# Optimization experiments

Hardware: AMD Instinct MI355X
Metric: run time of the kernel (lower is better)

The kernel has to match this reference:

```python
import jax, jax.numpy as jnp
import numpy as np

POOL = (7, 7)          # pool_size from init
CROP = (14, 14)        # crop_size = [p*2 for p in pool_size]


def setup_inputs() -> dict:
    key = jax.random.key(0)
    kf, kxy, kwh = jax.random.split(key, 3)
    H_img, W_img = 800, 800
    feature = jax.random.normal(kf, (1, 50, 50, 512), dtype=jnp.float32)
    N = 1024
    # valid boxes: x1<x2, y1<y2, inside the 800x800 image
    xy1 = jax.random.uniform(kxy, (N, 2), minval=0.0, maxval=600.0)
    wh = jax.random.uniform(kwh, (N, 2), minval=32.0, maxval=200.0)
    xy2 = jnp.clip(xy1 + wh, 0.0, 799.0)
    rois = jnp.concatenate([xy1[:, 0:1], xy1[:, 1:2], xy2[:, 0:1], xy2[:, 1:2]], axis=1)  # (x1,y1,x2,y2)
    img_size = jnp.array([H_img, W_img], dtype=jnp.int32)  # (H, W)
    return {"feature": feature, "rois": rois, "img_size": img_size}


def _roi_pool(feature, rois, img_size):
    H, W = feature.shape[1], feature.shape[2]
    ch, cw = CROP
    ih = img_size[0].astype(jnp.float32)
    iw = img_size[1].astype(jnp.float32)
    # normalize rois (x1,y1,x2,y2) by [W,H,W,H], reorder to (y1,x1,y2,x2)
    x1 = rois[:, 0] / iw
    y1 = rois[:, 1] / ih
    x2 = rois[:, 2] / iw
    y2 = rois[:, 3] / ih
    # TF crop_and_resize sampling grid (crop size > 1 branch)
    gy = jnp.arange(ch, dtype=jnp.float32)
    gx = jnp.arange(cw, dtype=jnp.float32)
    in_y = y1[:, None] * (H - 1) + gy[None, :] * ((y2 - y1) * (H - 1) / (ch - 1))[:, None]  # [N,ch]
    in_x = x1[:, None] * (W - 1) + gx[None, :] * ((x2 - x1) * (W - 1) / (cw - 1))[:, None]  # [N,cw]
    top = jnp.floor(in_y)
    left = jnp.floor(in_x)
    ly = in_y - top   # [N,ch]
    lx = in_x - left  # [N,cw]
    t = jnp.clip(top, 0, H - 1).astype(jnp.int32)
    b = jnp.clip(top + 1, 0, H - 1).astype(jnp.int32)
    l = jnp.clip(left, 0, W - 1).astype(jnp.int32)
    r = jnp.clip(left + 1, 0, W - 1).astype(jnp.int32)
    img = feature[0]  # box_ind is all zeros -> single image [H,W,C]
    tl = img[t[:, :, None], l[:, None, :]]  # [N,ch,cw,C]
    tr = img[t[:, :, None], r[:, None, :]]
    bl = img[b[:, :, None], l[:, None, :]]
    br = img[b[:, :, None], r[:, None, :]]
    lyE = ly[:, :, None, None]
    lxE = lx[:, None, :, None]
    crops = (tl * (1 - lyE) * (1 - lxE) + tr * (1 - lyE) * lxE
             + bl * lyE * (1 - lxE) + br * lyE * lxE)
    # extrapolation_value = 0 outside [0, dim-1]
    valid = (((in_y >= 0) & (in_y <= H - 1))[:, :, None]
             & ((in_x >= 0) & (in_x <= W - 1))[:, None, :])
    crops = jnp.where(valid[..., None], crops, 0.0)
    # 2x2 max pool, stride 2 (crop dims are even so SAME == VALID)
    N, C = crops.shape[0], crops.shape[-1]
    pooled = crops.reshape(N, ch // 2, 2, cw // 2, 2, C).max(axis=(2, 4))  # [N,7,7,C]
    return pooled


def reference(feature, rois, img_size):
    return _roi_pool(feature, rois, img_size)
```

## Files before the change

kernel.cpp:

```cpp
#include <hip/hip_runtime.h>

#define FH 50
#define FW 50
#define FC 512
#define NROI 1024
#define ROWBYTES (FW * FC * 4)
#define COLBYTES (FC * 4)

typedef float f4v __attribute__((ext_vector_type(4)));

__device__ __forceinline__ float uflane(float v) {
    return __int_as_float(__builtin_amdgcn_readfirstlane(__float_as_int(v)));
}

__device__ __forceinline__ float4 lerp4(float4 a, float4 b, float t) {
    float4 r;
    r.x = fmaf(t, b.x - a.x, a.x);
    r.y = fmaf(t, b.y - a.y, a.y);
    r.z = fmaf(t, b.z - a.z, a.z);
    r.w = fmaf(t, b.w - a.w, a.w);
    return r;
}

__device__ __forceinline__ float4 max44(float4 a, float4 b) {
    float4 r;
    r.x = fmaxf(a.x, b.x);
    r.y = fmaxf(a.y, b.y);
    r.z = fmaxf(a.z, b.z);
    r.w = fmaxf(a.w, b.w);
    return r;
}

__global__ __launch_bounds__(256, 6) void roi_pool_kernel(
    const float* __restrict__ feature,
    const float* __restrict__ rois,
    const int*   __restrict__ img_size,
    float*       __restrict__ out)
{
    int tid  = threadIdx.x;
    int wid  = (blockIdx.x * 256 + tid) >> 6;
    wid = __builtin_amdgcn_readfirstlane(wid);
    int lane = tid & 63;

    int n    = wid / 14;
    int rem  = wid - n * 14;
    int py   = rem >> 1;
    int half = rem & 1;

    float ih = (float)__builtin_amdgcn_readfirstlane(img_size[0]);
    float iw = (float)__builtin_amdgcn_readfirstlane(img_size[1]);
    const float* rp = rois + (size_t)n * 4;
    float x1 = uflane(rp[0]) / iw;
    float y1 = uflane(rp[1]) / ih;
    float x2 = uflane(rp[2]) / iw;
    float y2 = uflane(rp[3]) / ih;

    const float HM1 = 49.0f;
    float sy = (y2 - y1) * HM1 / 13.0f;
    float sx = (x2 - x1) * HM1 / 13.0f;
    float oy = y1 * HM1;
    float ox = x1 * HM1;

    float iy0 = oy + (float)(2 * py)     * sy;
    float iy1 = oy + (float)(2 * py + 1) * sy;
    float fy0 = floorf(iy0), fy1 = floorf(iy1);
    float ly0 = iy0 - fy0,   ly1 = iy1 - fy1;
    int t0 = __builtin_amdgcn_readfirstlane((int)fy0);
    int t1 = __builtin_amdgcn_readfirstlane((int)fy1);
    bool sameRows = (t1 == t0);

    const char* base = (const char*)feature + (size_t)half * 1024;
    const char* rT0 = base + (size_t)t0 * ROWBYTES;
    const char* rB0 = rT0 + ROWBYTES;
    const char* rT1 = base + (size_t)t1 * ROWBYTES;
    const char* rB1 = rT1 + ROWBYTES;

    int voff0;
    int curL = __builtin_amdgcn_readfirstlane((int)floorf(ox));
    voff0 = curL * COLBYTES + lane * 16;

    auto loadcol = [&](int vo, float4& V0, float4& V1) {
        float4 A = *reinterpret_cast<const float4*>(rT0 + vo);
        float4 B = *reinterpret_cast<const float4*>(rB0 + vo);
        V0 = lerp4(A, B, ly0);
        if (sameRows) {
            V1 = lerp4(A, B, ly1);
        } else {
            float4 C = *reinterpret_cast<const float4*>(rT1 + vo);
            float4 D = *reinterpret_cast<const float4*>(rB1 + vo);
            V1 = lerp4(C, D, ly1);
        }
    };

    float4 VA0, VA1, VB0, VB1;
    loadcol(voff0,            VA0, VA1);
    loadcol(voff0 + COLBYTES, VB0, VB1);
    int voffN = voff0 + 2 * COLBYTES;

    float* obase = out + ((size_t)n * 49 + (size_t)py * 7) * FC + half * 256 + lane * 4;

    float4 m;
#pragma unroll 2
    for (int j = 0; j < 14; ++j) {
        float ix = ox + (float)j * sx;
        float fx = floorf(ix);
        int   lj = (int)fx;
        float lx = ix - fx;
        while (lj > curL) {
            ++curL;
            VA0 = VB0; VA1 = VB1;
            loadcol(voffN, VB0, VB1);
            voffN += COLBYTES;
        }
        float4 s0 = lerp4(VA0, VB0, lx);
        float4 s1 = lerp4(VA1, VB1, lx);
        float4 sm = max44(s0, s1);
        if (j & 1) {
            m = max44(m, sm);
            __builtin_nontemporal_store(*reinterpret_cast<f4v*>(&m),
                reinterpret_cast<f4v*>(obase + (size_t)(j >> 1) * FC));
        } else {
            m = sm;
        }
    }
}

extern "C" void kernel_launch(void* const* d_in, const int* in_sizes, int n_in,
                              void* d_out, int out_size, void* d_ws, size_t ws_size,
                              hipStream_t stream) {
    const float* feature  = (const float*)d_in[0];
    const float* rois     = (const float*)d_in[1];
    const int*   img_size = (const int*)d_in[2];
    float* out = (float*)d_out;

    int blocks = NROI * 14 / 4;
    roi_pool_kernel<<<blocks, 256, 0, stream>>>(feature, rois, img_size, out);
}
```

Before: 33.03 us.

## Process two pooled rows per wave to share vertical row loads

Each wavefront now computes two pooled output rows (four crop sample rows) instead of one, reusing shared feature rows across consecutive sample rows through a sliding top/bottom register pair. This cuts redundant global loads of overlapping feature rows and halves the wave count, at the cost of more registers per thread (occupancy hint lowered from 6 to 5). The last group has only one real pooled row and recomputes clamped rows before skipping the second store, so some work is wasted there.

```diff
diff --git a/kernel.cpp b/kernel.cpp
--- a/kernel.cpp
+++ b/kernel.cpp
@@ -31,7 +31,7 @@
     return r;
 }
 
-__global__ __launch_bounds__(256, 6) void roi_pool_kernel(
+__global__ __launch_bounds__(256, 5) void roi_pool_kernel(
     const float* __restrict__ feature,
     const float* __restrict__ rois,
     const int*   __restrict__ img_size,
@@ -42,9 +42,9 @@
     wid = __builtin_amdgcn_readfirstlane(wid);
     int lane = tid & 63;
 
-    int n    = wid / 14;
-    int rem  = wid - n * 14;
-    int py   = rem >> 1;
+    int n    = wid >> 3;
+    int rem  = wid & 7;
+    int g    = rem >> 1;
     int half = rem & 1;
 
     float ih = (float)__builtin_amdgcn_readfirstlane(img_size[0]);
@@ -61,45 +61,56 @@
     float oy = y1 * HM1;
     float ox = x1 * HM1;
 
-    float iy0 = oy + (float)(2 * py)     * sy;
-    float iy1 = oy + (float)(2 * py + 1) * sy;
-    float fy0 = floorf(iy0), fy1 = floorf(iy1);
-    float ly0 = iy0 - fy0,   ly1 = iy1 - fy1;
+    int i0 = g * 4;
+    int s0i = i0, s1i = i0 + 1, s2i = min(i0 + 2, 13), s3i = min(i0 + 3, 13);
+    float iy0 = oy + (float)s0i * sy;
+    float iy1 = oy + (float)s1i * sy;
+    float iy2 = oy + (float)s2i * sy;
+    float iy3 = oy + (float)s3i * sy;
+    float fy0 = floorf(iy0), fy1 = floorf(iy1), fy2 = floorf(iy2), fy3 = floorf(iy3);
+    float ly0 = iy0 - fy0, ly1 = iy1 - fy1, ly2 = iy2 - fy2, ly3 = iy3 - fy3;
     int t0 = __builtin_amdgcn_readfirstlane((int)fy0);
     int t1 = __builtin_amdgcn_readfirstlane((int)fy1);
-    bool sameRows = (t1 == t0);
+    int t2 = __builtin_amdgcn_readfirstlane((int)fy2);
+    int t3 = __builtin_amdgcn_readfirstlane((int)fy3);
+    int adv1 = t1 - t0;
+    int adv2 = t2 - t1;
+    int adv3 = t3 - t2;
 
-    const char* base = (const char*)feature + (size_t)half * 1024;
-    const char* rT0 = base + (size_t)t0 * ROWBYTES;
-    const char* rB0 = rT0 + ROWBYTES;
-    const char* rT1 = base + (size_t)t1 * ROWBYTES;
-    const char* rB1 = rT1 + ROWBYTES;
+    const char* rT0 = (const char*)feature + (size_t)half * 1024
+                    + (size_t)t0 * ROWBYTES;
 
-    int voff0;
     int curL = __builtin_amdgcn_readfirstlane((int)floorf(ox));
-    voff0 = curL * COLBYTES + lane * 16;
+    int voff = curL * COLBYTES + lane * 16;
 
-    auto loadcol = [&](int vo, float4& V0, float4& V1) {
-        float4 A = *reinterpret_cast<const float4*>(rT0 + vo);
-        float4 B = *reinterpret_cast<const float4*>(rB0 + vo);
-        V0 = lerp4(A, B, ly0);
-        if (sameRows) {
-            V1 = lerp4(A, B, ly1);
-        } else {
-            float4 C = *reinterpret_cast<const float4*>(rT1 + vo);
-            float4 D = *reinterpret_cast<const float4*>(rB1 + vo);
-            V1 = lerp4(C, D, ly1);
-        }
-    };
+#define VERTCOL(vo, W0, W1, W2, W3)                                             \
+    {                                                                           \
+        const char* pB = rT0 + ROWBYTES;                                        \
+        float4 A = *reinterpret_cast<const float4*>(rT0 + (vo));                \
+        float4 B = *reinterpret_cast<const float4*>(pB + (vo));                 \
+        W0 = lerp4(A, B, ly0);                                                  \
+        if (adv1) { A = B; pB += ROWBYTES;                                      \
+                    B = *reinterpret_cast<const float4*>(pB + (vo)); }          \
+        W1 = lerp4(A, B, ly1);                                                  \
+        if (adv2) { A = B; pB += ROWBYTES;                                      \
+                    B = *reinterpret_cast<const float4*>(pB + (vo)); }          \
+        W2 = lerp4(A, B, ly2);                                                  \
+        if (adv3) { A = B; pB += ROWBYTES;                                      \
+                    B = *reinterpret_cast<const float4*>(pB + (vo)); }          \
+        W3 = lerp4(A, B, ly3);                                                  \
+    }
 
-    float4 VA0, VA1, VB0, VB1;
-    loadcol(voff0,            VA0, VA1);
-    loadcol(voff0 + COLBYTES, VB0, VB1);
-    int voffN = voff0 + 2 * COLBYTES;
+    float4 Vp0, Vp1, Vp2, Vp3, Vb0, Vb1, Vb2, Vb3;
+    VERTCOL(voff,            Vp0, Vp1, Vp2, Vp3);
+    VERTCOL(voff + COLBYTES, Vb0, Vb1, Vb2, Vb3);
+    int voffN = voff + 2 * COLBYTES;
 
-    float* obase = out + ((size_t)n * 49 + (size_t)py * 7) * FC + half * 256 + lane * 4;
+    float* ob0 = out + ((size_t)n * 49 + (size_t)(2 * g) * 7) * FC
+                     + half * 256 + lane * 4;
+    float* ob1 = ob0 + 7 * FC;
+    bool hasP1 = (g < 3);
 
-    float4 m;
+    float4 m01, m23;
 #pragma unroll 2
     for (int j = 0; j < 14; ++j) {
         float ix = ox + (float)j * sx;
@@ -108,21 +119,31 @@
         float lx = ix - fx;
         while (lj > curL) {
             ++curL;
-            VA0 = VB0; VA1 = VB1;
-            loadcol(voffN, VB0, VB1);
+            Vp0 = Vb0; Vp1 = Vb1; Vp2 = Vb2; Vp3 = Vb3;
+            VERTCOL(voffN, Vb0, Vb1, Vb2, Vb3);
             voffN += COLBYTES;
         }
-        float4 s0 = lerp4(VA0, VB0, lx);
-        float4 s1 = lerp4(VA1, VB1, lx);
-        float4 sm = max44(s0, s1);
+        float4 sA = lerp4(Vp0, Vb0, lx);
+        float4 sB = lerp4(Vp1, Vb1, lx);
+        float4 sC = lerp4(Vp2, Vb2, lx);
+        float4 sD = lerp4(Vp3, Vb3, lx);
+        float4 a = max44(sA, sB);
+        float4 b = max44(sC, sD);
         if (j & 1) {
-            m = max44(m, sm);
-            __builtin_nontemporal_store(*reinterpret_cast<f4v*>(&m),
-                reinterpret_cast<f4v*>(obase + (size_t)(j >> 1) * FC));
+            m01 = max44(m01, a);
+            m23 = max44(m23, b);
+            __builtin_nontemporal_store(*reinterpret_cast<f4v*>(&m01),
+                reinterpret_cast<f4v*>(ob0 + (size_t)(j >> 1) * FC));
+            if (hasP1) {
+                __builtin_nontemporal_store(*reinterpret_cast<f4v*>(&m23),
+                    reinterpret_cast<f4v*>(ob1 + (size_t)(j >> 1) * FC));
+            }
         } else {
-            m = sm;
+            m01 = a;
+            m23 = b;
         }
     }
+#undef VERTCOL
 }
 
 extern "C" void kernel_launch(void* const* d_in, const int* in_sizes, int n_in,
@@ -133,6 +154,6 @@
     const int*   img_size = (const int*)d_in[2];
     float* out = (float*)d_out;
 
-    int blocks = NROI * 14 / 4;
+    int blocks = NROI * 8 / 4;
     roi_pool_kernel<<<blocks, 256, 0, stream>>>(feature, rois, img_size, out);
 }
```

After: 57.53 us. 74.1% more time.
